# Optimization experiments

Measured on AMD Instinct MI355X. Metric: run time of the kernel, lower is better.

Reference implementation:

```python
import jax, jax.numpy as jnp
import numpy as np
from jax import lax

EPS = 1e-5
W_BITS = 8
A_BITS = 8


def _ste_round(x):
    # straight-through round (brevitas-style)
    return x + lax.stop_gradient(jnp.round(x) - x)


def weight_fake_quant(w, bits=W_BITS):
    # symmetric per-output-channel int quant: scale = max|w| / (2^(b-1)-1)
    qmax = float(2 ** (bits - 1) - 1)
    s = jnp.max(jnp.abs(w), axis=(1, 2, 3), keepdims=True) / qmax
    s = jnp.maximum(s, 1e-8)
    return jnp.clip(_ste_round(w / s), -qmax, qmax) * s


def quant_relu(x, scale, bits=A_BITS):
    # QuantReLU: relu then unsigned fake-quant with learned per-tensor scale
    qmax = float(2 ** bits - 1)
    s = jnp.maximum(scale, 1e-6)
    return jnp.clip(_ste_round(jax.nn.relu(x) / s), 0.0, qmax) * s


def conv2d(x, w, stride=1, padding=0):
    return lax.conv_general_dilated(
        x, w, window_strides=(stride, stride),
        padding=[(padding, padding), (padding, padding)],
        dimension_numbers=('NCHW', 'OIHW', 'NCHW'))


def batchnorm(x, gamma, beta, mean, var):
    # eval-mode BN with running stats
    inv = gamma / jnp.sqrt(var + EPS)
    return x * inv[None, :, None, None] + (beta - mean * inv)[None, :, None, None]


def setup_inputs() -> dict:
    key = jax.random.key(0)
    ks = jax.random.split(key, 20)
    B, Cin, P, H, W = 64, 1024, 256, 14, 14
    inp = {
        'x': jax.random.normal(ks[0], (B, Cin, H, W), jnp.float32),
        'w1': jax.random.normal(ks[1], (P, Cin, 1, 1), jnp.float32) * 0.05,
        'w2': jax.random.normal(ks[2], (P, P, 3, 3), jnp.float32) * 0.05,
        'w3': jax.random.normal(ks[3], (Cin, P, 1, 1), jnp.float32) * 0.05,
        'bn1_gamma': jax.random.uniform(ks[4], (P,), jnp.float32, 0.5, 1.5),
        'bn1_beta': jax.random.normal(ks[5], (P,), jnp.float32) * 0.1,
        'bn1_mean': jax.random.normal(ks[6], (P,), jnp.float32) * 0.1,
        'bn1_var': jax.random.uniform(ks[7], (P,), jnp.float32, 0.5, 1.5),
        'bn2_gamma': jax.random.uniform(ks[8], (P,), jnp.float32, 0.5, 1.5),
        'bn2_beta': jax.random.normal(ks[9], (P,), jnp.float32) * 0.1,
        'bn2_mean': jax.random.normal(ks[10], (P,), jnp.float32) * 0.1,
        'bn2_var': jax.random.uniform(ks[11], (P,), jnp.float32, 0.5, 1.5),
        'bn3_gamma': jax.random.uniform(ks[12], (Cin,), jnp.float32, 0.5, 1.5),
        'bn3_beta': jax.random.normal(ks[13], (Cin,), jnp.float32) * 0.1,
        'bn3_mean': jax.random.normal(ks[14], (Cin,), jnp.float32) * 0.1,
        'bn3_var': jax.random.uniform(ks[15], (Cin,), jnp.float32, 0.5, 1.5),
        's1': jax.random.uniform(ks[16], (1,), jnp.float32, 0.02, 0.1),
        's2': jax.random.uniform(ks[17], (1,), jnp.float32, 0.02, 0.1),
        's3': jax.random.uniform(ks[18], (1,), jnp.float32, 0.02, 0.1),
    }
    return inp


def reference(x, w1, w2, w3,
              bn1_gamma, bn1_beta, bn1_mean, bn1_var,
              bn2_gamma, bn2_beta, bn2_mean, bn2_var,
              bn3_gamma, bn3_beta, bn3_mean, bn3_var,
              s1, s2, s3):
    identity = x
    out = conv2d(x, weight_fake_quant(w1))
    out = batchnorm(out, bn1_gamma, bn1_beta, bn1_mean, bn1_var)
    out = quant_relu(out, s1)
    out = conv2d(out, weight_fake_quant(w2), stride=1, padding=1)
    out = batchnorm(out, bn2_gamma, bn2_beta, bn2_mean, bn2_var)
    out = quant_relu(out, s2)
    out = conv2d(out, weight_fake_quant(w3))
    out = batchnorm(out, bn3_gamma, bn3_beta, bn3_mean, bn3_var)
    out = out + identity  # downsample=None -> identity skip
    out = quant_relu(out, s3)
    return out
```

## Files before the change

### kernel.cpp

```cpp
#include <hip/hip_runtime.h>
#include <stdint.h>
#include <stddef.h>

typedef unsigned short u16;
typedef unsigned int   u32;
typedef __bf16  bf16x8 __attribute__((ext_vector_type(8)));
typedef unsigned short us8 __attribute__((ext_vector_type(8)));
typedef unsigned short us4 __attribute__((ext_vector_type(4)));
typedef float   f32x4  __attribute__((ext_vector_type(4)));

#define DEVFN static __device__ __forceinline__

DEVFN u16 f2bf(float f) {
    u32 u = __float_as_uint(f);
    return (u16)((u + 0x7FFFu + ((u >> 16) & 1u)) >> 16);
}
DEVFN float bf2f(u16 h) { return __uint_as_float(((u32)h) << 16); }

#define GLL(g, l) __builtin_amdgcn_global_load_lds( \
    (__attribute__((address_space(1))) void*)(g),   \
    (__attribute__((address_space(3))) void*)(l), 16, 0, 0)

#define NREAL 12544
#define NPAD  16384
#define GUARD_ROWS 32

DEVFN float blockReduceMax(float m) {
    for (int off = 32; off; off >>= 1) m = fmaxf(m, __shfl_xor(m, off));
    __shared__ float s[4];
    int lane = threadIdx.x & 63, w = threadIdx.x >> 6;
    if (lane == 0) s[w] = m;
    __syncthreads();
    m = fmaxf(fmaxf(s[0], s[1]), fmaxf(s[2], s[3]));
    return m;
}

__global__ void k_wq1(const float* __restrict__ w1, u16* __restrict__ w1d, float* __restrict__ sw1) {
    int p = blockIdx.x, t = threadIdx.x;
    const float* wr = w1 + (size_t)p * 1024;
    float v[4], m = 0.f;
    for (int i = 0; i < 4; ++i) { v[i] = wr[t + i*256]; m = fmaxf(m, fabsf(v[i])); }
    m = blockReduceMax(m);
    float s = fmaxf(m / 127.0f, 1e-8f);
    if (t == 0) sw1[p] = s;
    for (int i = 0; i < 4; ++i) {
        float q = rintf(v[i] / s);
        q = fminf(fmaxf(q, -127.f), 127.f);
        u16 h = f2bf(q);
        w1d[(size_t)p*2048 + t + i*256]        = h;
        w1d[(size_t)p*2048 + 1024 + t + i*256] = h;
    }
}

__global__ void k_wq2(const float* __restrict__ w2, u16* __restrict__ w2t, float* __restrict__ sw2) {
    int p = blockIdx.x, t = threadIdx.x;
    const float* wr = w2 + (size_t)p * 2304;
    float v[9], m = 0.f;
    for (int i = 0; i < 9; ++i) { v[i] = wr[t + i*256]; m = fmaxf(m, fabsf(v[i])); }
    m = blockReduceMax(m);
    float s = fmaxf(m / 127.0f, 1e-8f);
    if (t == 0) sw2[p] = s;
    for (int i = 0; i < 9; ++i) {
        int f = t + i*256;
        int ci = f / 9, r = f - ci*9;
        float q = rintf(v[i] / s);
        q = fminf(fmaxf(q, -127.f), 127.f);
        w2t[(size_t)p*2304 + r*256 + ci] = f2bf(q);
    }
}

__global__ void k_wq3(const float* __restrict__ w3, u16* __restrict__ w3q, float* __restrict__ sw3) {
    int co = blockIdx.x, t = threadIdx.x;
    float v = w3[(size_t)co*256 + t];
    float m = blockReduceMax(fabsf(v));
    float s = fmaxf(m / 127.0f, 1e-8f);
    if (t == 0) sw3[co] = s;
    float q = rintf(v / s);
    q = fminf(fmaxf(q, -127.f), 127.f);
    w3q[(size_t)co*256 + t] = f2bf(q);
}

__global__ void k_coef(const float* g1, const float* b1, const float* m1, const float* v1,
                       const float* g2, const float* b2, const float* m2, const float* v2,
                       const float* g3, const float* b3, const float* m3, const float* v3,
                       const float* s1p, const float* s2p,
                       const float* sw1, const float* sw2, const float* sw3,
                       float* a1, float* c1, float* a2, float* c2, float* a3, float* c3) {
    int t = threadIdx.x;
    float s1 = fmaxf(s1p[0], 1e-6f), s2 = fmaxf(s2p[0], 1e-6f);
    if (t < 256) {
        float inv1 = g1[t] / sqrtf(v1[t] + 1e-5f);
        a1[t] = sw1[t] * inv1 / s1;
        c1[t] = (b1[t] - m1[t] * inv1) / s1;
        float inv2 = g2[t] / sqrtf(v2[t] + 1e-5f);
        a2[t] = sw2[t] * s1 * inv2 / s2;
        c2[t] = (b2[t] - m2[t] * inv2) / s2;
    }
    float inv3 = g3[t] / sqrtf(v3[t] + 1e-5f);
    a3[t] = sw3[t] * s2 * inv3;
    c3[t] = b3[t] - m3[t] * inv3;
}

__global__ void k_split(const float* __restrict__ x, u16* __restrict__ xsplit) {
    __shared__ float tile[64*197];
    int b = blockIdx.x >> 4, cg = blockIdx.x & 15;
    int t = threadIdx.x;
    const float* xb = x + ((size_t)b*1024 + cg*64) * 196;
    for (int i = t; i < 3136; i += 256) {
        f32x4 v = *(const f32x4*)&xb[i*4];
        int g = i*4;
#pragma unroll
        for (int j = 0; j < 4; ++j) {
            int gg = g + j;
            tile[gg + gg/196] = v[j];
        }
    }
    __syncthreads();
    for (int i = t; i < 3136; i += 256) {
        int pos = i >> 4, c4 = (i & 15) << 2;
        us4 hi, lo;
#pragma unroll
        for (int j = 0; j < 4; ++j) {
            float v = tile[(c4 + j)*197 + pos];
            u16 h = f2bf(v);
            hi[j] = h;
            lo[j] = f2bf(v - bf2f(h));
        }
        size_t n = (size_t)(b*196 + pos);
        *(us4*)&xsplit[n*2048 + cg*64 + c4]        = hi;
        *(us4*)&xsplit[n*2048 + 1024 + cg*64 + c4] = lo;
    }
}

template<int CONV>
__global__ __launch_bounds__(256) void k_gemm(
    const u16* __restrict__ A, const u16* __restrict__ Bact,
    u16* __restrict__ actout,
    const float* __restrict__ ca, const float* __restrict__ cc,
    const float* __restrict__ xin, const float* __restrict__ s3p,
    float* __restrict__ outp)
{
    constexpr int KSA = CONV==1 ? 2048 : (CONV==2 ? 2304 : 256);
    constexpr int KSB = CONV==1 ? 2048 : 256;
    constexpr int NKT = CONV==1 ? 32 : (CONV==2 ? 36 : 4);

    __shared__ u16 lA[128*64];
    __shared__ u16 lB[64*64];

    const int t = threadIdx.x;
    const int lane = t & 63, wv = t >> 6;
    const int n0 = blockIdx.x * 64, m0 = blockIdx.y * 128;

    f32x4 acc[4][2];
#pragma unroll
    for (int i = 0; i < 4; ++i)
#pragma unroll
        for (int j = 0; j < 2; ++j) acc[i][j] = f32x4{0.f,0.f,0.f,0.f};

    const int srA = wv*32 + (lane >> 3);
    const int srB = wv*16 + (lane >> 3);
    const int ssel = (((lane & 7) ^ ((lane >> 3) & 7))) * 8;
    const int wr = wv >> 1, wc = wv & 1;
    const int fr = lane & 15, fg = lane >> 4;
    const int fsw = (fr & 7) << 4;

    for (int kt = 0; kt < NKT; ++kt) {
        int bcol, bshift;
        if constexpr (CONV == 2) {
            bcol = (kt & 3) * 64;
            int kpos = kt >> 2;
            int ky = kpos / 3, kx = kpos - ky*3;
            bshift = (ky - 1)*16 + (kx - 1);
        } else { bcol = kt * 64; bshift = 0; }

#pragma unroll
        for (int c = 0; c < 4; ++c) {
            const u16* g = A + (size_t)(m0 + srA + c*8) * KSA + kt*64 + ssel;
            GLL(g, &lA[(wv*32 + c*8) * 64]);
        }
#pragma unroll
        for (int c = 0; c < 2; ++c) {
            const u16* g = Bact + (ptrdiff_t)(n0 + srB + c*8 + bshift) * KSB + bcol + ssel;
            GLL(g, &lB[(wv*16 + c*8) * 64]);
        }
        __syncthreads();

#pragma unroll
        for (int kk = 0; kk < 2; ++kk) {
            bf16x8 af[4], bfv[2];
#pragma unroll
            for (int m = 0; m < 4; ++m) {
                int row = wr*64 + m*16 + fr;
                const char* p = (const char*)lA + row*128 + ((kk*64 + fg*16) ^ fsw);
                af[m] = __builtin_bit_cast(bf16x8, *(const us8*)p);
            }
#pragma unroll
            for (int n = 0; n < 2; ++n) {
                int row = wc*32 + n*16 + fr;
                const char* p = (const char*)lB + row*128 + ((kk*64 + fg*16) ^ fsw);
                bfv[n] = __builtin_bit_cast(bf16x8, *(const us8*)p);
            }
#pragma unroll
            for (int m = 0; m < 4; ++m)
#pragma unroll
                for (int n = 0; n < 2; ++n)
                    acc[m][n] = __builtin_amdgcn_mfma_f32_16x16x32_bf16(af[m], bfv[n], acc[m][n], 0, 0, 0);
        }
        __syncthreads();
    }

    const int pb = m0 + wr*64 + fg*4;
    const int nb = n0 + wc*32 + fr;

    if constexpr (CONV != 3) {
        (void)xin; (void)s3p; (void)outp;
#pragma unroll
        for (int m = 0; m < 4; ++m) {
            int p0 = pb + m*16;
            float av[4], cv[4];
#pragma unroll
            for (int j = 0; j < 4; ++j) { av[j] = ca[p0+j]; cv[j] = cc[p0+j]; }
#pragma unroll
            for (int n = 0; n < 2; ++n) {
                int nn = nb + n*16;
                int np;
                if constexpr (CONV == 1) {
                    int b  = nn / 196;
                    int pos = nn - b*196;
                    int h = pos / 14, w = pos - h*14;
                    np = b*256 + (h+1)*16 + (w+1);
                } else {
                    int hp = (nn >> 4) & 15, wp = nn & 15;
                    if (hp < 1 || hp > 14 || wp < 1 || wp > 14) continue;
                    np = (nn >> 8)*196 + (hp-1)*14 + (wp-1);
                }
                us4 st;
#pragma unroll
                for (int j = 0; j < 4; ++j) {
                    float y = fmaxf(acc[m][n][j]*av[j] + cv[j], 0.f);
                    float q = fminf(rintf(y), 255.f);
                    st[j] = f2bf(q);
                }
                *(us4*)&actout[(size_t)np*256 + p0] = st;
            }
        }
    } else {
        (void)actout;
        float s3 = fmaxf(s3p[0], 1e-6f);
        float rs3 = 1.0f / s3;
#pragma unroll
        for (int n = 0; n < 2; ++n) {
            int co = nb + n*16;
            float av = ca[co], cv = cc[co];
#pragma unroll
            for (int m = 0; m < 4; ++m) {
                int p4 = pb + m*16;
                int b  = p4 / 196;
                int hw = p4 - b*196;
                size_t off = ((size_t)((b << 10) + co))*196 + hw;
                f32x4 xv = *(const f32x4*)&xin[off];
                f32x4 st;
#pragma unroll
                for (int j = 0; j < 4; ++j) {
                    float y = fmaxf(acc[m][n][j]*av + cv + xv[j], 0.f);
                    float q = fminf(rintf(y * rs3), 255.f);
                    st[j] = q * s3;
                }
                *(f32x4*)&outp[off] = st;
            }
        }
    }
}

extern "C" void kernel_launch(void* const* d_in, const int* in_sizes, int n_in,
                              void* d_out, int out_size, void* d_ws, size_t ws_size,
                              hipStream_t stream) {
    (void)in_sizes; (void)n_in; (void)out_size; (void)ws_size;
    const float* x   = (const float*)d_in[0];
    const float* w1  = (const float*)d_in[1];
    const float* w2  = (const float*)d_in[2];
    const float* w3  = (const float*)d_in[3];
    const float* g1  = (const float*)d_in[4];
    const float* b1  = (const float*)d_in[5];
    const float* m1  = (const float*)d_in[6];
    const float* v1  = (const float*)d_in[7];
    const float* g2  = (const float*)d_in[8];
    const float* b2  = (const float*)d_in[9];
    const float* m2  = (const float*)d_in[10];
    const float* v2  = (const float*)d_in[11];
    const float* g3  = (const float*)d_in[12];
    const float* b3  = (const float*)d_in[13];
    const float* m3  = (const float*)d_in[14];
    const float* v3  = (const float*)d_in[15];
    const float* s1p = (const float*)d_in[16];
    const float* s2p = (const float*)d_in[17];
    const float* s3p = (const float*)d_in[18];
    float* out = (float*)d_out;

    char* w = (char*)d_ws;
    u16* w1d = (u16*)w;  w += (size_t)256*2048*2;
    u16* w2t = (u16*)w;  w += (size_t)256*2304*2;
    u16* w3q = (u16*)w;  w += (size_t)1024*256*2;
    float* sw1 = (float*)w; w += 256*4;
    float* sw2 = (float*)w; w += 256*4;
    float* sw3 = (float*)w; w += 1024*4;
    float* a1 = (float*)w; w += 256*4;
    float* c1 = (float*)w; w += 256*4;
    float* a2 = (float*)w; w += 256*4;
    float* c2 = (float*)w; w += 256*4;
    float* a3 = (float*)w; w += 1024*4;
    float* c3 = (float*)w; w += 1024*4;
    u16* xsplit = (u16*)w; w += (size_t)NREAL*2048*2;
    u16* act1g  = (u16*)w; w += (size_t)(NPAD + 2*GUARD_ROWS)*256*2;
    u16* act1   = act1g + (size_t)GUARD_ROWS*256;
    u16* act2   = (u16*)w; w += (size_t)NREAL*256*2;

    hipMemsetAsync(act1g, 0, (size_t)(NPAD + 2*GUARD_ROWS)*256*2, stream);

    k_wq1<<<256, 256, 0, stream>>>(w1, w1d, sw1);
    k_wq2<<<256, 256, 0, stream>>>(w2, w2t, sw2);
    k_wq3<<<1024, 256, 0, stream>>>(w3, w3q, sw3);
    k_coef<<<1, 1024, 0, stream>>>(g1,b1,m1,v1, g2,b2,m2,v2, g3,b3,m3,v3,
                                   s1p, s2p, sw1, sw2, sw3,
                                   a1,c1, a2,c2, a3,c3);
    k_split<<<1024, 256, 0, stream>>>(x, xsplit);

    k_gemm<1><<<dim3(196, 2), 256, 0, stream>>>(w1d, xsplit, act1, a1, c1, nullptr, nullptr, nullptr);
    k_gemm<2><<<dim3(256, 2), 256, 0, stream>>>(w2t, act1, act2, a2, c2, nullptr, nullptr, nullptr);
    k_gemm<3><<<dim3(16, 98), 256, 0, stream>>>(act2, w3q, nullptr, a3, c3, x, s3p, out);
}
```

Baseline: 243.6 us.

## Triple-buffer GEMM K-loop with async LDS loads and merge prep kernels

The GEMM main loop now uses three LDS buffers and issues global-to-LDS loads two K-tiles ahead. Each step waits with a partial vmcnt and a single barrier instead of two full syncthreads, so memory latency overlaps with MFMA work. The three weight-quant kernels and the input split kernel are also merged into one launch to cut launch overhead and let them run concurrently. This triples GEMM LDS usage (72KB per block), which may lower occupancy, and the merged prep kernel allocates the tile shared memory in every block.

```diff
diff --git a/kernel.cpp b/kernel.cpp
--- a/kernel.cpp
+++ b/kernel.cpp
@@ -35,49 +35,84 @@
     return m;
 }
 
-__global__ void k_wq1(const float* __restrict__ w1, u16* __restrict__ w1d, float* __restrict__ sw1) {
-    int p = blockIdx.x, t = threadIdx.x;
-    const float* wr = w1 + (size_t)p * 1024;
-    float v[4], m = 0.f;
-    for (int i = 0; i < 4; ++i) { v[i] = wr[t + i*256]; m = fmaxf(m, fabsf(v[i])); }
-    m = blockReduceMax(m);
-    float s = fmaxf(m / 127.0f, 1e-8f);
-    if (t == 0) sw1[p] = s;
-    for (int i = 0; i < 4; ++i) {
-        float q = rintf(v[i] / s);
+__global__ __launch_bounds__(256) void k_prep(
+    const float* __restrict__ w1, const float* __restrict__ w2, const float* __restrict__ w3,
+    const float* __restrict__ x,
+    u16* __restrict__ w1d, u16* __restrict__ w2t, u16* __restrict__ w3q,
+    float* __restrict__ sw1, float* __restrict__ sw2, float* __restrict__ sw3,
+    u16* __restrict__ xsplit)
+{
+    __shared__ float tile[64*197];
+    const int bid = blockIdx.x, t = threadIdx.x;
+
+    if (bid < 256) {
+        int p = bid;
+        const float* wr = w1 + (size_t)p * 1024;
+        float v[4], m = 0.f;
+        for (int i = 0; i < 4; ++i) { v[i] = wr[t + i*256]; m = fmaxf(m, fabsf(v[i])); }
+        m = blockReduceMax(m);
+        float s = fmaxf(m / 127.0f, 1e-8f);
+        if (t == 0) sw1[p] = s;
+        for (int i = 0; i < 4; ++i) {
+            float q = rintf(v[i] / s);
+            q = fminf(fmaxf(q, -127.f), 127.f);
+            u16 h = f2bf(q);
+            w1d[(size_t)p*2048 + t + i*256]        = h;
+            w1d[(size_t)p*2048 + 1024 + t + i*256] = h;
+        }
+    } else if (bid < 512) {
+        int p = bid - 256;
+        const float* wr = w2 + (size_t)p * 2304;
+        float v[9], m = 0.f;
+        for (int i = 0; i < 9; ++i) { v[i] = wr[t + i*256]; m = fmaxf(m, fabsf(v[i])); }
+        m = blockReduceMax(m);
+        float s = fmaxf(m / 127.0f, 1e-8f);
+        if (t == 0) sw2[p] = s;
+        for (int i = 0; i < 9; ++i) {
+            int f = t + i*256;
+            int ci = f / 9, r = f - ci*9;
+            float q = rintf(v[i] / s);
+            q = fminf(fmaxf(q, -127.f), 127.f);
+            w2t[(size_t)p*2304 + r*256 + ci] = f2bf(q);
+        }
+    } else if (bid < 1536) {
+        int co = bid - 512;
+        float v = w3[(size_t)co*256 + t];
+        float m = blockReduceMax(fabsf(v));
+        float s = fmaxf(m / 127.0f, 1e-8f);
+        if (t == 0) sw3[co] = s;
+        float q = rintf(v / s);
         q = fminf(fmaxf(q, -127.f), 127.f);
-        u16 h = f2bf(q);
-        w1d[(size_t)p*2048 + t + i*256]        = h;
-        w1d[(size_t)p*2048 + 1024 + t + i*256] = h;
+        w3q[(size_t)co*256 + t] = f2bf(q);
+    } else {
+        int sb = bid - 1536;
+        int b = sb >> 4, cg = sb & 15;
+        const float* xb = x + ((size_t)b*1024 + cg*64) * 196;
+        for (int i = t; i < 3136; i += 256) {
+            f32x4 v = *(const f32x4*)&xb[i*4];
+            int g = i*4;
+#pragma unroll
+            for (int j = 0; j < 4; ++j) {
+                int gg = g + j;
+                tile[gg + gg/196] = v[j];
+            }
+        }
+        __syncthreads();
+        for (int i = t; i < 3136; i += 256) {
+            int pos = i >> 4, c4 = (i & 15) << 2;
+            us4 hi, lo;
+#pragma unroll
+            for (int j = 0; j < 4; ++j) {
+                float v = tile[(c4 + j)*197 + pos];
+                u16 h = f2bf(v);
+                hi[j] = h;
+                lo[j] = f2bf(v - bf2f(h));
+            }
+            size_t n = (size_t)(b*196 + pos);
+            *(us4*)&xsplit[n*2048 + cg*64 + c4]        = hi;
+            *(us4*)&xsplit[n*2048 + 1024 + cg*64 + c4] = lo;
+        }
     }
-}
-
-__global__ void k_wq2(const float* __restrict__ w2, u16* __restrict__ w2t, float* __restrict__ sw2) {
-    int p = blockIdx.x, t = threadIdx.x;
-    const float* wr = w2 + (size_t)p * 2304;
-    float v[9], m = 0.f;
-    for (int i = 0; i < 9; ++i) { v[i] = wr[t + i*256]; m = fmaxf(m, fabsf(v[i])); }
-    m = blockReduceMax(m);
-    float s = fmaxf(m / 127.0f, 1e-8f);
-    if (t == 0) sw2[p] = s;
-    for (int i = 0; i < 9; ++i) {
-        int f = t + i*256;
-        int ci = f / 9, r = f - ci*9;
-        float q = rintf(v[i] / s);
-        q = fminf(fmaxf(q, -127.f), 127.f);
-        w2t[(size_t)p*2304 + r*256 + ci] = f2bf(q);
-    }
-}
-
-__global__ void k_wq3(const float* __restrict__ w3, u16* __restrict__ w3q, float* __restrict__ sw3) {
-    int co = blockIdx.x, t = threadIdx.x;
-    float v = w3[(size_t)co*256 + t];
-    float m = blockReduceMax(fabsf(v));
-    float s = fmaxf(m / 127.0f, 1e-8f);
-    if (t == 0) sw3[co] = s;
-    float q = rintf(v / s);
-    q = fminf(fmaxf(q, -127.f), 127.f);
-    w3q[(size_t)co*256 + t] = f2bf(q);
 }
 
 __global__ void k_coef(const float* g1, const float* b1, const float* m1, const float* v1,
@@ -101,37 +136,6 @@
     c3[t] = b3[t] - m3[t] * inv3;
 }
 
-__global__ void k_split(const float* __restrict__ x, u16* __restrict__ xsplit) {
-    __shared__ float tile[64*197];
-    int b = blockIdx.x >> 4, cg = blockIdx.x & 15;
-    int t = threadIdx.x;
-    const float* xb = x + ((size_t)b*1024 + cg*64) * 196;
-    for (int i = t; i < 3136; i += 256) {
-        f32x4 v = *(const f32x4*)&xb[i*4];
-        int g = i*4;
-#pragma unroll
-        for (int j = 0; j < 4; ++j) {
-            int gg = g + j;
-            tile[gg + gg/196] = v[j];
-        }
-    }
-    __syncthreads();
-    for (int i = t; i < 3136; i += 256) {
-        int pos = i >> 4, c4 = (i & 15) << 2;
-        us4 hi, lo;
-#pragma unroll
-        for (int j = 0; j < 4; ++j) {
-            float v = tile[(c4 + j)*197 + pos];
-            u16 h = f2bf(v);
-            hi[j] = h;
-            lo[j] = f2bf(v - bf2f(h));
-        }
-        size_t n = (size_t)(b*196 + pos);
-        *(us4*)&xsplit[n*2048 + cg*64 + c4]        = hi;
-        *(us4*)&xsplit[n*2048 + 1024 + cg*64 + c4] = lo;
-    }
-}
-
 template<int CONV>
 __global__ __launch_bounds__(256) void k_gemm(
     const u16* __restrict__ A, const u16* __restrict__ Bact,
@@ -144,8 +148,8 @@
     constexpr int KSB = CONV==1 ? 2048 : 256;
     constexpr int NKT = CONV==1 ? 32 : (CONV==2 ? 36 : 4);
 
-    __shared__ u16 lA[128*64];
-    __shared__ u16 lB[64*64];
+    __shared__ u16 lA[3][128*64];
+    __shared__ u16 lB[3][64*64];
 
     const int t = threadIdx.x;
     const int lane = t & 63, wv = t >> 6;
@@ -164,7 +168,7 @@
     const int fr = lane & 15, fg = lane >> 4;
     const int fsw = (fr & 7) << 4;
 
-    for (int kt = 0; kt < NKT; ++kt) {
+    auto stageK = [&](int kt, int buf) {
         int bcol, bshift;
         if constexpr (CONV == 2) {
             bcol = (kt & 3) * 64;
@@ -172,32 +176,35 @@
             int ky = kpos / 3, kx = kpos - ky*3;
             bshift = (ky - 1)*16 + (kx - 1);
         } else { bcol = kt * 64; bshift = 0; }
-
 #pragma unroll
         for (int c = 0; c < 4; ++c) {
             const u16* g = A + (size_t)(m0 + srA + c*8) * KSA + kt*64 + ssel;
-            GLL(g, &lA[(wv*32 + c*8) * 64]);
+            GLL(g, &lA[buf][(wv*32 + c*8) * 64]);
         }
 #pragma unroll
         for (int c = 0; c < 2; ++c) {
             const u16* g = Bact + (ptrdiff_t)(n0 + srB + c*8 + bshift) * KSB + bcol + ssel;
-            GLL(g, &lB[(wv*16 + c*8) * 64]);
-        }
-        __syncthreads();
-
+            GLL(g, &lB[buf][(wv*16 + c*8) * 64]);
+        }
+    };
+
+    auto computeK = [&](int buf) {
+        const char* bA = (const char*)&lA[buf][0];
+        const char* bB = (const char*)&lB[buf][0];
+        __builtin_amdgcn_s_setprio(1);
 #pragma unroll
         for (int kk = 0; kk < 2; ++kk) {
             bf16x8 af[4], bfv[2];
 #pragma unroll
             for (int m = 0; m < 4; ++m) {
                 int row = wr*64 + m*16 + fr;
-                const char* p = (const char*)lA + row*128 + ((kk*64 + fg*16) ^ fsw);
+                const char* p = bA + row*128 + ((kk*64 + fg*16) ^ fsw);
                 af[m] = __builtin_bit_cast(bf16x8, *(const us8*)p);
             }
 #pragma unroll
             for (int n = 0; n < 2; ++n) {
                 int row = wc*32 + n*16 + fr;
-                const char* p = (const char*)lB + row*128 + ((kk*64 + fg*16) ^ fsw);
+                const char* p = bB + row*128 + ((kk*64 + fg*16) ^ fsw);
                 bfv[n] = __builtin_bit_cast(bf16x8, *(const us8*)p);
             }
 #pragma unroll
@@ -206,7 +213,25 @@
                 for (int n = 0; n < 2; ++n)
                     acc[m][n] = __builtin_amdgcn_mfma_f32_16x16x32_bf16(af[m], bfv[n], acc[m][n], 0, 0, 0);
         }
-        __syncthreads();
+        __builtin_amdgcn_s_setprio(0);
+    };
+
+    stageK(0, 0);
+    stageK(1, 1);
+    asm volatile("s_waitcnt vmcnt(6)" ::: "memory");
+    __builtin_amdgcn_s_barrier();
+
+    int cur = 0;
+    for (int kt = 0; kt < NKT; ++kt) {
+        int nxt2 = cur + 2; if (nxt2 >= 3) nxt2 -= 3;
+        if (kt + 2 < NKT) stageK(kt + 2, nxt2);
+        computeK(cur);
+        if (kt + 1 < NKT) {
+            if (kt + 2 < NKT) { asm volatile("s_waitcnt vmcnt(6)" ::: "memory"); }
+            else              { asm volatile("s_waitcnt vmcnt(0)" ::: "memory"); }
+            __builtin_amdgcn_s_barrier();
+        }
+        cur = cur + 1 == 3 ? 0 : cur + 1;
     }
 
     const int pb = m0 + wr*64 + fg*4;
@@ -317,13 +342,10 @@
 
     hipMemsetAsync(act1g, 0, (size_t)(NPAD + 2*GUARD_ROWS)*256*2, stream);
 
-    k_wq1<<<256, 256, 0, stream>>>(w1, w1d, sw1);
-    k_wq2<<<256, 256, 0, stream>>>(w2, w2t, sw2);
-    k_wq3<<<1024, 256, 0, stream>>>(w3, w3q, sw3);
+    k_prep<<<2560, 256, 0, stream>>>(w1, w2, w3, x, w1d, w2t, w3q, sw1, sw2, sw3, xsplit);
     k_coef<<<1, 1024, 0, stream>>>(g1,b1,m1,v1, g2,b2,m2,v2, g3,b3,m3,v3,
                                    s1p, s2p, sw1, sw2, sw3,
                                    a1,c1, a2,c2, a3,c3);
-    k_split<<<1024, 256, 0, stream>>>(x, xsplit);
 
     k_gemm<1><<<dim3(196, 2), 256, 0, stream>>>(w1d, xsplit, act1, a1, c1, nullptr, nullptr, nullptr);
     k_gemm<2><<<dim3(256, 2), 256, 0, stream>>>(w2t, act1, act2, a2, c2, nullptr, nullptr, nullptr);
```

Measured after the change: 250.2 us. +2.7%, slower.
